# Performance work log

Hardware: AMD Instinct MI355X
Metric: run time of the kernel (lower is better)

Reference implementation:

```python
import jax, jax.numpy as jnp
import numpy as np

B, V, J, NB = 512, 6890, 24, 10
P = (J - 1) * 9  # 207 pose-blendshape features
# Standard SMPL kinematic tree (parents[0] = -1 for root)
PARENTS = np.array([-1, 0, 0, 0, 1, 2, 3, 4, 5, 6, 7, 8, 9, 9, 9, 12, 13, 14, 16, 17, 18, 19, 20, 21])


def rodrigues(aa):
    """Axis-angle [N,3] -> rotation matrices [N,3,3] (batch_rodrigues)."""
    angle = jnp.linalg.norm(aa, axis=-1, keepdims=True) + 1e-8
    axis = aa / angle
    x, y, z = axis[..., 0], axis[..., 1], axis[..., 2]
    zero = jnp.zeros_like(x)
    K = jnp.stack([zero, -z, y, z, zero, -x, -y, x, zero], axis=-1).reshape(aa.shape[0], 3, 3)
    s = jnp.sin(angle)[..., None]
    c = jnp.cos(angle)[..., None]
    return jnp.eye(3, dtype=aa.dtype) + s * K + (1.0 - c) * jnp.matmul(K, K)


def setup_inputs() -> dict:
    key = jax.random.key(0)
    ks = jax.random.split(key, 9)
    J_reg = jax.random.uniform(ks[7], (J, V), dtype=jnp.float32)
    J_reg = J_reg / jnp.sum(J_reg, axis=1, keepdims=True)
    W = jax.nn.softmax(4.0 * jax.random.normal(ks[8], (V, J), dtype=jnp.float32), axis=-1)
    return {
        "betas": jax.random.normal(ks[0], (B, NB), dtype=jnp.float32),
        "body_pose": 0.3 * jax.random.normal(ks[1], (B, (J - 1) * 3), dtype=jnp.float32),
        "global_orient": 0.3 * jax.random.normal(ks[2], (B, 3), dtype=jnp.float32),
        "transl": jax.random.normal(ks[3], (B, 3), dtype=jnp.float32),
        "v_template": jax.random.normal(ks[4], (V, 3), dtype=jnp.float32),
        "shapedirs": 0.01 * jax.random.normal(ks[5], (V, 3, NB), dtype=jnp.float32),
        "posedirs": 0.01 * jax.random.normal(ks[6], (P, V * 3), dtype=jnp.float32),
        "J_regressor": J_reg,
        "lbs_weights": W,
    }


def reference(betas, body_pose, global_orient, transl, v_template, shapedirs, posedirs, J_regressor, lbs_weights):
    b = betas.shape[0]
    # --- pose to rotation matrices (pose2rot=True path) ---
    full_pose = jnp.concatenate([global_orient, body_pose], axis=-1)  # [B, 72]
    rot_mats = rodrigues(full_pose.reshape(-1, 3)).reshape(b, J, 3, 3)
    # --- shape blend shapes ---
    v_shaped = v_template + jnp.einsum('bl,vcl->bvc', betas, shapedirs)  # [B,V,3]
    joints = jnp.einsum('jv,bvc->bjc', J_regressor, v_shaped)            # [B,J,3]
    # --- pose blend shapes ---
    pose_feature = (rot_mats[:, 1:] - jnp.eye(3, dtype=rot_mats.dtype)).reshape(b, P)
    v_posed = v_shaped + (pose_feature @ posedirs).reshape(b, V, 3)
    # --- kinematic chain (batch_rigid_transform) ---
    rel_joints = joints.at[:, 1:].add(-joints[:, PARENTS[1:]])
    top = jnp.concatenate([rot_mats, rel_joints[..., None]], axis=-1)   # [B,J,3,4]
    bottom = jnp.broadcast_to(jnp.array([0.0, 0.0, 0.0, 1.0], dtype=rot_mats.dtype), (b, J, 1, 4))
    mats = jnp.concatenate([top, bottom], axis=-2)                      # [B,J,4,4]
    chain = [mats[:, 0]]
    for i in range(1, J):  # fixed 24-joint serial composition
        chain.append(chain[PARENTS[i]] @ mats[:, i])
    A = jnp.stack(chain, axis=1)                                        # [B,J,4,4]
    posed_joints = A[..., :3, 3]
    # remove rest-pose joint locations from the transforms
    t_rel = A[..., :3, 3] - jnp.einsum('bjmn,bjn->bjm', A[..., :3, :3], joints)
    A_rel = A.at[..., :3, 3].set(t_rel)
    # --- linear blend skinning ---
    T = jnp.einsum('vj,bjmn->bvmn', lbs_weights, A_rel)                 # [B,V,4,4]
    verts = jnp.einsum('bvmn,bvn->bvm', T[..., :3, :3], v_posed) + T[..., :3, 3]
    vertices = verts + transl[:, None]
    joints_out = posed_joints + transl[:, None]
    return vertices, joints_out
```

## Files before the change

### kernel.cpp

```cpp
#include <hip/hip_runtime.h>
#include <hip/hip_bf16.h>
#include <math.h>

#define Bn 512
#define Vn 6890
#define NBn 10
#define Pn 207
#define N3n 20670
#define KP 224
#define VPAD 6912

typedef __attribute__((ext_vector_type(8))) _Float16 half8;
typedef __attribute__((ext_vector_type(4))) float f32x4;

__constant__ int c_par[24] = {-1,0,0,0,1,2,3,4,5,6,7,8,9,9,9,12,13,14,16,17,18,19,20,21};
__constant__ int c_lvl[10] = {0,1,4,7,10,15,18,20,22,24};


__global__ __launch_bounds__(256) void k_prep(
    const float* __restrict__ Jreg, const float* __restrict__ vtpl,
    const float* __restrict__ sdirs, const float* __restrict__ pdirs,
    const float* __restrict__ W, float* __restrict__ part,
    _Float16* __restrict__ B_h, _Float16* __restrict__ W_h)
{
  const int tid = threadIdx.x;
  __shared__ float wred[4][33];
  __shared__ __align__(16) float tile[224][36];

  if (blockIdx.x < 192) {
    const int j = blockIdx.x % 24;
    const int chunk = blockIdx.x / 24;
    const int lane = tid & 63, wv = tid >> 6;
    const int vlo = chunk * 862;
    const int vhi = min(Vn, vlo + 862);
    float acc[33];
#pragma unroll
    for (int k = 0; k < 33; k++) acc[k] = 0.f;
    for (int v = vlo + tid; v < vhi; v += 256) {
      float w = Jreg[(size_t)j * Vn + v];
      const float* sp = sdirs + (size_t)v * 30;
#pragma unroll
      for (int c = 0; c < 3; c++) {
#pragma unroll
        for (int l = 0; l < 10; l++) acc[c*11 + l] += w * sp[c*10 + l];
        acc[c*11 + 10] += w * vtpl[v*3 + c];
      }
    }
#pragma unroll
    for (int k = 0; k < 33; k++) {
      float s = acc[k];
      for (int off = 32; off > 0; off >>= 1) s += __shfl_xor(s, off);
      if (lane == 0) wred[wv][k] = s;
    }
    __syncthreads();
    if (tid < 33) {
      float s = wred[0][tid] + wred[1][tid] + wred[2][tid] + wred[3][tid];
      int c = tid / 11, k = tid % 11;
      part[(size_t)chunk * 792 + (j*3 + c) * 11 + k] = s;
    }
  } else if (blockIdx.x < 840) {
    const int p = blockIdx.x - 192;
    const int cols0 = p * 32;
    for (int idx = tid; idx < 207 * 8; idx += 256) {
      int row = idx >> 3, cq = (idx & 7) << 2;
      int gc = cols0 + cq;
      float4 v4 = {0.f, 0.f, 0.f, 0.f};
      if (gc + 3 < N3n) {
        v4 = *(const float4*)(pdirs + (size_t)row * N3n + gc);
      } else if (gc < N3n) {
        float t[4];
#pragma unroll
        for (int e = 0; e < 4; e++) t[e] = (gc + e < N3n) ? pdirs[(size_t)row * N3n + gc + e] : 0.f;
        v4 = make_float4(t[0], t[1], t[2], t[3]);
      }
      *(float4*)&tile[row][cq] = v4;
    }
    for (int idx = tid; idx < 17 * 32; idx += 256) {
      int r = idx >> 5, cc = idx & 31;
      int k = 207 + r;
      int gc = cols0 + cc;
      float f = 0.f;
      if (gc < N3n) {
        if (k < 217)      f = sdirs[(size_t)gc * 10 + (k - 207)];
        else if (k == 217) f = (float)(_Float16)vtpl[gc];
        else if (k == 218) { float tv = vtpl[gc]; f = tv - (float)(_Float16)tv; }
      }
      tile[k][cc] = f;
    }
    __syncthreads();
    for (int idx = tid; idx < 896; idx += 256) {
      int pl = idx >> 6;
      int l  = idx & 63;
      int ntl = pl / 7, s = pl % 7;
      int colc = ntl * 16 + (l & 15);
      int kb = s * 32 + ((l >> 4) << 3);
      half8 hv;
#pragma unroll
      for (int j = 0; j < 8; j++) hv[j] = (_Float16)tile[kb + j][colc];
      *(half8*)(B_h + ((size_t)(2 * p + ntl) * 7 + s) * 512 + (size_t)l * 8) = hv;
    }
  } else {
    int idx = (blockIdx.x - 840) * 256 + tid;
    if (idx < VPAD * 32) {
      int v = idx >> 5, k = idx & 31;
      float f;
      if (v < Vn && k < 24) f = W[(size_t)v * 24 + k];
      else if (k == 24)     f = 1.0f;
      else                  f = 0.f;
      W_h[idx] = (_Float16)f;
    }
  }
}

__global__ __launch_bounds__(256) void k_pose2(
    const float* __restrict__ betas, const float* __restrict__ body_pose,
    const float* __restrict__ gorient, const float* __restrict__ transl,
    const float* __restrict__ part,
    _Float16* __restrict__ pf_h, _Float16* __restrict__ Ar_h,
    float* __restrict__ out_joints)
{
  const int tid = threadIdx.x;
  const int wave = tid >> 6;
  const int lane = tid & 63;
  const int b = blockIdx.x * 4 + wave;

  __shared__ float JS_s[720];
  __shared__ float Jt_s[72];
  __shared__ float Rs[4][24][9];
  __shared__ float jnt[4][24][3];
  __shared__ float rel[4][24][3];
  __shared__ float A_s[4][24][12];

  for (int idx = tid; idx < 792; idx += 256) {
    float s = 0.f;
#pragma unroll
    for (int y = 0; y < 8; y++) s += part[(size_t)y * 792 + idx];
    int bid = idx / 11, k = idx % 11;
    if (k < 10) JS_s[bid * 10 + k] = s;
    else        Jt_s[bid] = s;
  }

  if (lane < 24) {
    float x, y, z;
    if (lane == 0) { x = gorient[b*3+0]; y = gorient[b*3+1]; z = gorient[b*3+2]; }
    else { int o = b*69 + (lane-1)*3; x = body_pose[o]; y = body_pose[o+1]; z = body_pose[o+2]; }
    float ang = sqrtf(x*x + y*y + z*z) + 1e-8f;
    float inv = 1.0f / ang;
    float ux = x*inv, uy = y*inv, uz = z*inv;
    float s = sinf(ang), cc = cosf(ang), omc = 1.0f - cc;
    float K[9] = {0.f, -uz, uy,  uz, 0.f, -ux,  -uy, ux, 0.f};
#pragma unroll
    for (int mm = 0; mm < 3; mm++)
#pragma unroll
      for (int nn = 0; nn < 3; nn++) {
        float kk = K[mm*3+0]*K[0+nn] + K[mm*3+1]*K[3+nn] + K[mm*3+2]*K[6+nn];
        float eye = (mm == nn) ? 1.0f : 0.0f;
        Rs[wave][lane][mm*3+nn] = eye + s*K[mm*3+nn] + omc*kk;
      }
  }
  __syncthreads();

  for (int idx = lane; idx < 72; idx += 64) {
    float a = Jt_s[idx];
#pragma unroll
    for (int l = 0; l < 10; l++) a += betas[b*10 + l] * JS_s[idx*10 + l];
    jnt[wave][idx/3][idx%3] = a;
  }
  for (int idx = lane; idx < KP; idx += 64) {
    float f = 0.f;
    if (idx < Pn) {
      int j = 1 + idx / 9, e = idx % 9;
      float eye = (e == 0 || e == 4 || e == 8) ? 1.0f : 0.0f;
      f = Rs[wave][j][e] - eye;
    } else if (idx < 217) {
      f = betas[b*10 + (idx - 207)];
    } else if (idx < 219) {
      f = 1.0f;
    }
    pf_h[(size_t)b * KP + idx] = (_Float16)f;
  }
  __syncthreads();
  for (int idx = lane; idx < 72; idx += 64) {
    int j = idx/3, cc = idx%3;
    float r = jnt[wave][j][cc];
    if (j > 0) r -= jnt[wave][c_par[j]][cc];
    rel[wave][j][cc] = r;
  }
  __syncthreads();
  if (lane < 12) {
    int m = lane/4, nn = lane%4;
    A_s[wave][0][lane] = (nn < 3) ? Rs[wave][0][m*3+nn] : rel[wave][0][m];
  }
  __syncthreads();
  for (int lev = 1; lev <= 8; lev++) {
    const int s0 = c_lvl[lev], s1 = c_lvl[lev + 1];
    const int jj = lane / 12, r = lane % 12;
    if (jj < s1 - s0) {
      const int i = s0 + jj;
      const int p = c_par[i];
      const int m = r >> 2, nn = r & 3;
      float v;
      if (nn < 3)
        v = A_s[wave][p][m*4+0]*Rs[wave][i][0+nn] + A_s[wave][p][m*4+1]*Rs[wave][i][3+nn] + A_s[wave][p][m*4+2]*Rs[wave][i][6+nn];
      else
        v = A_s[wave][p][m*4+0]*rel[wave][i][0] + A_s[wave][p][m*4+1]*rel[wave][i][1] + A_s[wave][p][m*4+2]*rel[wave][i][2] + A_s[wave][p][m*4+3];
      A_s[wave][i][r] = v;
    }
    __syncthreads();
  }
  for (int idx = lane; idx < 72; idx += 64) {
    int j = idx/3, cc = idx%3;
    out_joints[(size_t)b * 72 + idx] = A_s[wave][j][cc*4+3] + transl[b*3+cc];
  }
  for (int idx = lane; idx < 512; idx += 64) {
    int e = idx >> 5, k = idx & 31;
    float a = 0.f;
    if (e < 12 && k < 24) {
      int m = e >> 2, nn = e & 3;
      if (nn < 3) a = A_s[wave][k][m*4+nn];
      else a = A_s[wave][k][m*4+3] - (A_s[wave][k][m*4+0]*jnt[wave][k][0] + A_s[wave][k][m*4+1]*jnt[wave][k][1] + A_s[wave][k][m*4+2]*jnt[wave][k][2]);
    } else if (k == 24 && e < 12 && (e & 3) == 3) {
      a = transl[b*3 + (e >> 2)];
    }
    Ar_h[(size_t)b * 512 + idx] = (_Float16)a;
  }
}

__global__ __launch_bounds__(256) void k_mm5(
    const _Float16* __restrict__ pf_h, const _Float16* __restrict__ B_h,
    const _Float16* __restrict__ W_h, const _Float16* __restrict__ Ar_h,
    float* __restrict__ out)
{
  const int lin = blockIdx.x;
  const int r8 = lin & 7;
  const int k2 = lin >> 3;
  const int b_t = k2 & 15;
  const int m8 = k2 >> 4;
  const int v_t = r8 * 14 + m8;
  if (v_t >= 108) return;

  const int tid = threadIdx.x;
  const int l = tid & 63;
  const int wave = tid >> 6;
  const int b0 = b_t * 32;
  const int v0 = v_t * 64;

  __shared__ __align__(16) float vpT[192 * 32];

  const int c0 = l & 15;
  const int kk0 = (l >> 4) << 3;
  const int ntb = v_t * 12 + wave * 3;
  f32x4 acc[2][3];
#pragma unroll
  for (int t = 0; t < 2; t++)
#pragma unroll
    for (int n = 0; n < 3; n++) acc[t][n] = (f32x4){0.f, 0.f, 0.f, 0.f};

#pragma unroll
  for (int s = 0; s < 7; s++) {
    half8 bv[3];
#pragma unroll
    for (int n = 0; n < 3; n++)
      bv[n] = *(const half8*)(B_h + ((size_t)(ntb + n) * 7 + s) * 512 + l * 8);
#pragma unroll
    for (int t = 0; t < 2; t++) {
      half8 fa = *(const half8*)(pf_h + (size_t)(b0 + t * 16 + c0) * KP + kk0 + s * 32);
#pragma unroll
      for (int n = 0; n < 3; n++)
        acc[t][n] = __builtin_amdgcn_mfma_f32_16x16x32_f16(fa, bv[n], acc[t][n], 0, 0, 0);
    }
  }
  {
    const int rowq = (l >> 4) * 4;
#pragma unroll
    for (int t = 0; t < 2; t++)
#pragma unroll
      for (int n = 0; n < 3; n++) {
        const int col = wave * 48 + n * 16 + c0;
        const int rowb = t * 16 + rowq;
        *(f32x4*)&vpT[col * 32 + (rowb ^ ((col & 7) << 2))] = acc[t][n];
      }
  }
  __syncthreads();

  const int c = c0;
  const int g = l >> 4;
  const int kk = g << 3;

  half8 wh[4], ah[8];
#pragma unroll
  for (int mt = 0; mt < 4; mt++)
    wh[mt] = *(const half8*)(W_h + (size_t)(v0 + mt * 16 + c) * 32 + kk);
#pragma unroll
  for (int i = 0; i < 8; i++)
    ah[i] = *(const half8*)(Ar_h + (size_t)(b0 + wave * 8 + i) * 512 + c * 32 + kk);

#pragma unroll
  for (int mt = 0; mt < 4; mt++) {
    const int vl2 = mt * 16 + c;
    const int v = v0 + vl2;
    const bool ok = (g < 3) && (v < Vn);
    const int colx = 3 * vl2, coly = colx + 1, colz = colx + 2;
#pragma unroll
    for (int q = 0; q < 2; q++) {
      const int rb = wave * 8 + q * 4;
      f32x4 X = *(const f32x4*)&vpT[colx * 32 + (rb ^ ((colx & 7) << 2))];
      f32x4 Y = *(const f32x4*)&vpT[coly * 32 + (rb ^ ((coly & 7) << 2))];
      f32x4 Z = *(const f32x4*)&vpT[colz * 32 + (rb ^ ((colz & 7) << 2))];
#pragma unroll
      for (int r = 0; r < 4; r++) {
        f32x4 t = {0.f, 0.f, 0.f, 0.f};
        t = __builtin_amdgcn_mfma_f32_16x16x32_f16(ah[q * 4 + r], wh[mt], t, 0, 0, 0);
        if (ok) {
          const int bl = wave * 8 + q * 4 + r;
          out[((size_t)(b0 + bl) * Vn + v) * 3 + g] = t[0]*X[r] + t[1]*Y[r] + t[2]*Z[r] + t[3];
        }
      }
    }
  }
}


__global__ __launch_bounds__(256) void k_jsjt_part(
    const float* __restrict__ Jreg, const float* __restrict__ vtpl,
    const float* __restrict__ sdirs, float* __restrict__ part)
{
  const int bid = blockIdx.x;
  const int chunk = blockIdx.y;
  const int j = bid / 3, c = bid % 3;
  const int tid = threadIdx.x;
  const int vlo = chunk * 862;
  const int vhi = min(Vn, vlo + 862);
  float acc[11];
#pragma unroll
  for (int k = 0; k < 11; k++) acc[k] = 0.f;
  for (int v = vlo + tid; v < vhi; v += 256) {
    float w = Jreg[(size_t)j * Vn + v];
    int n = v * 3 + c;
#pragma unroll
    for (int l = 0; l < 10; l++) acc[l] += w * sdirs[(size_t)n * 10 + l];
    acc[10] += w * vtpl[n];
  }
  __shared__ float red[256];
  for (int k = 0; k < 11; k++) {
    red[tid] = acc[k];
    __syncthreads();
    for (int s = 128; s > 0; s >>= 1) {
      if (tid < s) red[tid] += red[tid + s];
      __syncthreads();
    }
    if (tid == 0) part[(size_t)chunk * 792 + bid * 11 + k] = red[0];
    __syncthreads();
  }
}

__global__ __launch_bounds__(1024) void k_jsjt_red(
    const float* __restrict__ part, float* __restrict__ JS, float* __restrict__ Jt)
{
  const int t = threadIdx.x;
  if (t >= 792) return;
  float s = 0.f;
#pragma unroll
  for (int y = 0; y < 8; y++) s += part[(size_t)y * 792 + t];
  int bid = t / 11, k = t % 11;
  if (k < 10) JS[bid * 10 + k] = s;
  else        Jt[bid] = s;
}

__global__ __launch_bounds__(64) void k_pose_fb(
    const float* __restrict__ betas, const float* __restrict__ body_pose,
    const float* __restrict__ gorient, const float* __restrict__ transl,
    const float* __restrict__ JS, const float* __restrict__ Jt,
    float* __restrict__ pf_ws, float* __restrict__ Ar_ws,
    float* __restrict__ out_joints)
{
  const int b = blockIdx.x;
  const int tid = threadIdx.x;
  __shared__ float Rs[24][9];
  __shared__ float jnt[24][3];
  __shared__ float rel[24][3];
  __shared__ float A_s[24][12];

  if (tid < 24) {
    float x, y, z;
    if (tid == 0) { x = gorient[b*3+0]; y = gorient[b*3+1]; z = gorient[b*3+2]; }
    else { int o = b*69 + (tid-1)*3; x = body_pose[o]; y = body_pose[o+1]; z = body_pose[o+2]; }
    float ang = sqrtf(x*x + y*y + z*z) + 1e-8f;
    float inv = 1.0f / ang;
    float ux = x*inv, uy = y*inv, uz = z*inv;
    float s = sinf(ang), cc = cosf(ang), omc = 1.0f - cc;
    float K[9] = {0.f, -uz, uy,  uz, 0.f, -ux,  -uy, ux, 0.f};
#pragma unroll
    for (int mm = 0; mm < 3; mm++)
#pragma unroll
      for (int nn = 0; nn < 3; nn++) {
        float kk = K[mm*3+0]*K[0+nn] + K[mm*3+1]*K[3+nn] + K[mm*3+2]*K[6+nn];
        float eye = (mm == nn) ? 1.0f : 0.0f;
        Rs[tid][mm*3+nn] = eye + s*K[mm*3+nn] + omc*kk;
      }
  }
  for (int idx = tid; idx < 72; idx += 64) {
    float a = Jt[idx];
#pragma unroll
    for (int l = 0; l < 10; l++) a += betas[b*10 + l] * JS[idx*10 + l];
    jnt[idx/3][idx%3] = a;
  }
  __syncthreads();
  for (int idx = tid; idx < Pn; idx += 64) {
    int j = 1 + idx / 9, e = idx % 9;
    float eye = (e == 0 || e == 4 || e == 8) ? 1.0f : 0.0f;
    pf_ws[(size_t)b * Pn + idx] = Rs[j][e] - eye;
  }
  for (int idx = tid; idx < 72; idx += 64) {
    int j = idx/3, cc = idx%3;
    float r = jnt[j][cc];
    if (j > 0) r -= jnt[c_par[j]][cc];
    rel[j][cc] = r;
  }
  __syncthreads();
  if (tid < 12) {
    int m = tid/4, nn = tid%4;
    A_s[0][tid] = (nn < 3) ? Rs[0][m*3+nn] : rel[0][m];
  }
  __syncthreads();
  for (int i = 1; i < 24; i++) {
    if (tid < 12) {
      int m = tid/4, nn = tid%4;
      int p = c_par[i];
      float v;
      if (nn < 3)
        v = A_s[p][m*4+0]*Rs[i][0+nn] + A_s[p][m*4+1]*Rs[i][3+nn] + A_s[p][m*4+2]*Rs[i][6+nn];
      else
        v = A_s[p][m*4+0]*rel[i][0] + A_s[p][m*4+1]*rel[i][1] + A_s[p][m*4+2]*rel[i][2] + A_s[p][m*4+3];
      A_s[i][tid] = v;
    }
    __syncthreads();
  }
  for (int idx = tid; idx < 72; idx += 64) {
    int j = idx/3, cc = idx%3;
    out_joints[(size_t)b * 72 + idx] = A_s[j][cc*4+3] + transl[b*3+cc];
  }
  for (int idx = tid; idx < 288; idx += 64) {
    int j = idx/12, r = idx%12, m = r/4, nn = r%4;
    float v;
    if (nn < 3) v = A_s[j][m*4+nn];
    else v = A_s[j][m*4+3] - (A_s[j][m*4+0]*jnt[j][0] + A_s[j][m*4+1]*jnt[j][1] + A_s[j][m*4+2]*jnt[j][2]);
    Ar_ws[(size_t)b * 288 + idx] = v;
  }
}

__global__ __launch_bounds__(192) void k_verts_fb(
    const float* __restrict__ betas, const float* __restrict__ transl,
    const float* __restrict__ vtpl, const float* __restrict__ sdirs,
    const float* __restrict__ pdirs, const float* __restrict__ W,
    const float* __restrict__ pf_ws, const float* __restrict__ Ar_ws,
    float* __restrict__ out)
{
  const int tid = threadIdx.x;
  const int b0 = blockIdx.x * 16;
  const int v0 = blockIdx.y * 128;
  const int n0 = v0 * 3;
  __shared__ __align__(16) float pf_s[Pn][16];
  __shared__ __align__(16) float Ar_s[16][288];
  __shared__ __align__(16) float vp_s[16][384];
  __shared__ float betas_s[16][NBn];
  __shared__ float transl_s[16][3];
  for (int idx = tid; idx < Pn * 16; idx += 192) {
    int p = idx >> 4, bi = idx & 15;
    pf_s[p][bi] = pf_ws[(size_t)(b0 + bi) * Pn + p];
  }
  for (int idx = tid; idx < 16 * 288; idx += 192)
    Ar_s[idx / 288][idx % 288] = Ar_ws[(size_t)b0 * 288 + idx];
  for (int idx = tid; idx < 16 * NBn; idx += 192)
    betas_s[idx / NBn][idx % NBn] = betas[(size_t)b0 * NBn + idx];
  for (int idx = tid; idx < 48; idx += 192)
    transl_s[idx / 3][idx % 3] = transl[(size_t)b0 * 3 + idx];
  __syncthreads();
  const int n = n0 + 2 * tid;
  const bool valid = (n < N3n);
  float acc0[16], acc1[16];
#pragma unroll
  for (int i = 0; i < 16; i++) { acc0[i] = 0.f; acc1[i] = 0.f; }
  for (int p = 0; p < Pn; p++) {
    float pd0 = 0.f, pd1 = 0.f;
    if (valid) { float2 t = *(const float2*)(pdirs + (size_t)p * N3n + n); pd0 = t.x; pd1 = t.y; }
    const float4* row = (const float4*)(pf_s[p]);
#pragma unroll
    for (int q = 0; q < 4; q++) {
      float4 f = row[q];
      acc0[4*q+0] += f.x * pd0;  acc1[4*q+0] += f.x * pd1;
      acc0[4*q+1] += f.y * pd0;  acc1[4*q+1] += f.y * pd1;
      acc0[4*q+2] += f.z * pd0;  acc1[4*q+2] += f.z * pd1;
      acc0[4*q+3] += f.w * pd0;  acc1[4*q+3] += f.w * pd1;
    }
  }
  float sd0[10], sd1[10], vt0 = 0.f, vt1 = 0.f;
#pragma unroll
  for (int l = 0; l < 10; l++) { sd0[l] = 0.f; sd1[l] = 0.f; }
  if (valid) {
    for (int l = 0; l < 10; l++) { sd0[l] = sdirs[(size_t)n*10 + l]; sd1[l] = sdirs[(size_t)n*10 + 10 + l]; }
    vt0 = vtpl[n]; vt1 = vtpl[n+1];
  }
#pragma unroll
  for (int bi = 0; bi < 16; bi++) {
    float s0 = vt0, s1 = vt1;
#pragma unroll
    for (int l = 0; l < 10; l++) { float bb = betas_s[bi][l]; s0 += bb*sd0[l]; s1 += bb*sd1[l]; }
    acc0[bi] += s0; acc1[bi] += s1;
  }
#pragma unroll
  for (int bi = 0; bi < 16; bi++) { vp_s[bi][2*tid] = acc0[bi]; vp_s[bi][2*tid+1] = acc1[bi]; }
  __syncthreads();
  const int m = tid / 64;
  const int vl = tid % 64;
  const int va = v0 + vl, vb = v0 + vl + 64;
  const bool va_ok = (va < Vn), vb_ok = (vb < Vn);
  float Wr0[24], Wr1[24];
#pragma unroll
  for (int j = 0; j < 24; j++) { Wr0[j] = 0.f; Wr1[j] = 0.f; }
  if (va_ok) { const float4* wp = (const float4*)(W + (size_t)va*24);
#pragma unroll
    for (int q = 0; q < 6; q++) { float4 f = wp[q]; Wr0[4*q]=f.x; Wr0[4*q+1]=f.y; Wr0[4*q+2]=f.z; Wr0[4*q+3]=f.w; } }
  if (vb_ok) { const float4* wp = (const float4*)(W + (size_t)vb*24);
#pragma unroll
    for (int q = 0; q < 6; q++) { float4 f = wp[q]; Wr1[4*q]=f.x; Wr1[4*q+1]=f.y; Wr1[4*q+2]=f.z; Wr1[4*q+3]=f.w; } }
  for (int bi = 0; bi < 16; bi++) {
    float Ta0=0.f,Ta1=0.f,Ta2=0.f,Ta3=0.f, Tb0=0.f,Tb1=0.f,Tb2=0.f,Tb3=0.f;
    const float4* arb = (const float4*)(Ar_s[bi]);
#pragma unroll
    for (int j = 0; j < 24; j++) {
      float4 a = arb[j*3 + m];
      float wa = Wr0[j], wb = Wr1[j];
      Ta0 += wa*a.x; Ta1 += wa*a.y; Ta2 += wa*a.z; Ta3 += wa*a.w;
      Tb0 += wb*a.x; Tb1 += wb*a.y; Tb2 += wb*a.z; Tb3 += wb*a.w;
    }
    float tr = transl_s[bi][m];
    if (va_ok) {
      float x = vp_s[bi][vl*3+0], y = vp_s[bi][vl*3+1], z = vp_s[bi][vl*3+2];
      out[((size_t)(b0+bi)*Vn + va)*3 + m] = Ta0*x + Ta1*y + Ta2*z + Ta3 + tr;
    }
    if (vb_ok) {
      float x = vp_s[bi][(vl+64)*3+0], y = vp_s[bi][(vl+64)*3+1], z = vp_s[bi][(vl+64)*3+2];
      out[((size_t)(b0+bi)*Vn + vb)*3 + m] = Tb0*x + Tb1*y + Tb2*z + Tb3 + tr;
    }
  }
}

extern "C" void kernel_launch(void* const* d_in, const int* in_sizes, int n_in,
                              void* d_out, int out_size, void* d_ws, size_t ws_size,
                              hipStream_t stream)
{
  const float *betas=nullptr, *bpose=nullptr, *gorient=nullptr, *transl=nullptr,
              *vtpl=nullptr, *sdirs=nullptr, *pdirs=nullptr, *Jreg=nullptr, *W=nullptr;
  int seen1536 = 0, seen165360 = 0;
  for (int i = 0; i < n_in; i++) {
    const float* p = (const float*)d_in[i];
    switch (in_sizes[i]) {
      case 5120:    betas = p; break;
      case 35328:   bpose = p; break;
      case 20670:   vtpl  = p; break;
      case 206700:  sdirs = p; break;
      case 4278690: pdirs = p; break;
      case 1536:    if (seen1536++ == 0) gorient = p; else transl = p; break;
      case 165360:  if (seen165360++ == 0) Jreg = p; else W = p; break;
      default: break;
    }
  }
  float* out = (float*)d_out;

  float* ws   = (float*)d_ws;
  float* part = ws;
  float* JS   = ws + 6336;
  float* Jt   = ws + 7056;
  float* pf   = ws + 7128;
  float* Ar   = ws + 113112;
  _Float16* pf_h = (_Float16*)(ws + 260568);
  _Float16* B_h  = (_Float16*)(ws + 317912);
  _Float16* W_h  = (_Float16*)(ws + 2640344);
  _Float16* Ar_h = (_Float16*)(ws + 2861528);
  const size_t WS_NEED = (size_t)3123672 * 4;
  const bool big = (ws_size >= WS_NEED);

  if (big) {
    k_prep<<<1704, 256, 0, stream>>>(Jreg, vtpl, sdirs, pdirs, W, part, B_h, W_h);
    k_pose2<<<128, 256, 0, stream>>>(betas, bpose, gorient, transl, part,
                                     pf_h, Ar_h, out + (size_t)Bn * Vn * 3);
    k_mm5<<<1792, 256, 0, stream>>>(pf_h, B_h, W_h, Ar_h, out);
  } else {
    k_jsjt_part<<<dim3(72, 8), 256, 0, stream>>>(Jreg, vtpl, sdirs, part);
    k_jsjt_red<<<1, 1024, 0, stream>>>(part, JS, Jt);
    k_pose_fb<<<Bn, 64, 0, stream>>>(betas, bpose, gorient, transl, JS, Jt, pf, Ar,
                                     out + (size_t)Bn * Vn * 3);
    k_verts_fb<<<dim3(32, 54), 192, 0, stream>>>(betas, transl, vtpl, sdirs,
                                                 pdirs, W, pf, Ar, out);
  }
}
```

Baseline: 53.32 us.

## Repack skinning transforms so each MFMA covers four batches and drops padding rows

The per-batch fp16 skinning-transform matrix is now laid out in groups of four batches, ordered by output row m, with 4 batches × 4 columns packed into each 16-row MFMA operand. The old layout used 16 rows, of which only 12 were real and the g==3 lanes were masked. Each skinning MFMA now yields three useful output components (m loop) across four batches, and no quarter of the lanes is wasted. The goal is fewer MFMAs and Ar loads in the LBS epilogue and fewer idle lanes, at the cost of scalar LDS reads of vertex positions and a new index mapping that must stay consistent between producer and consumer.

```diff
diff --git a/kernel.cpp b/kernel.cpp
--- a/kernel.cpp
+++ b/kernel.cpp
@@ -212,21 +212,22 @@
     int j = idx/3, cc = idx%3;
     out_joints[(size_t)b * 72 + idx] = A_s[wave][j][cc*4+3] + transl[b*3+cc];
   }
-  for (int idx = lane; idx < 512; idx += 64) {
-    int e = idx >> 5, k = idx & 31;
+  for (int idx = lane; idx < 384; idx += 64) {
+    int m = idx >> 7;
+    int j = (idx >> 5) & 3;
+    int k = idx & 31;
     float a = 0.f;
-    if (e < 12 && k < 24) {
-      int m = e >> 2, nn = e & 3;
-      if (nn < 3) a = A_s[wave][k][m*4+nn];
+    if (k < 24) {
+      if (j < 3) a = A_s[wave][k][m*4+j];
       else a = A_s[wave][k][m*4+3] - (A_s[wave][k][m*4+0]*jnt[wave][k][0] + A_s[wave][k][m*4+1]*jnt[wave][k][1] + A_s[wave][k][m*4+2]*jnt[wave][k][2]);
-    } else if (k == 24 && e < 12 && (e & 3) == 3) {
-      a = transl[b*3 + (e >> 2)];
-    }
-    Ar_h[(size_t)b * 512 + idx] = (_Float16)a;
-  }
-}
-
-__global__ __launch_bounds__(256) void k_mm5(
+    } else if (k == 24 && j == 3) {
+      a = transl[b*3 + m];
+    }
+    Ar_h[(size_t)(b >> 2) * 1536 + m * 512 + ((b & 3) * 4 + j) * 32 + k] = (_Float16)a;
+  }
+}
+
+__global__ __launch_bounds__(256) void k_mm7(
     const _Float16* __restrict__ pf_h, const _Float16* __restrict__ B_h,
     const _Float16* __restrict__ W_h, const _Float16* __restrict__ Ar_h,
     float* __restrict__ out)
@@ -283,38 +284,41 @@
   }
   __syncthreads();
 
-  const int c = c0;
   const int g = l >> 4;
   const int kk = g << 3;
 
-  half8 wh[4], ah[8];
+  half8 wh[4];
 #pragma unroll
   for (int mt = 0; mt < 4; mt++)
-    wh[mt] = *(const half8*)(W_h + (size_t)(v0 + mt * 16 + c) * 32 + kk);
-#pragma unroll
-  for (int i = 0; i < 8; i++)
-    ah[i] = *(const half8*)(Ar_h + (size_t)(b0 + wave * 8 + i) * 512 + c * 32 + kk);
+    wh[mt] = *(const half8*)(W_h + (size_t)(v0 + mt * 16 + c0) * 32 + kk);
+
+  half8 aq[2][3];
+#pragma unroll
+  for (int q2 = 0; q2 < 2; q2++) {
+    const size_t qb = (size_t)(b_t * 8 + wave * 2 + q2) * 1536;
+#pragma unroll
+    for (int m = 0; m < 3; m++)
+      aq[q2][m] = *(const half8*)(Ar_h + qb + m * 512 + c0 * 32 + kk);
+  }
 
 #pragma unroll
   for (int mt = 0; mt < 4; mt++) {
-    const int vl2 = mt * 16 + c;
+    const int vl2 = mt * 16 + c0;
     const int v = v0 + vl2;
-    const bool ok = (g < 3) && (v < Vn);
+    const bool ok = (v < Vn);
     const int colx = 3 * vl2, coly = colx + 1, colz = colx + 2;
 #pragma unroll
-    for (int q = 0; q < 2; q++) {
-      const int rb = wave * 8 + q * 4;
-      f32x4 X = *(const f32x4*)&vpT[colx * 32 + (rb ^ ((colx & 7) << 2))];
-      f32x4 Y = *(const f32x4*)&vpT[coly * 32 + (rb ^ ((coly & 7) << 2))];
-      f32x4 Z = *(const f32x4*)&vpT[colz * 32 + (rb ^ ((colz & 7) << 2))];
-#pragma unroll
-      for (int r = 0; r < 4; r++) {
+    for (int q2 = 0; q2 < 2; q2++) {
+      const int bl = wave * 8 + q2 * 4 + g;
+      float x = vpT[colx * 32 + (bl ^ ((colx & 7) << 2))];
+      float y = vpT[coly * 32 + (bl ^ ((coly & 7) << 2))];
+      float z = vpT[colz * 32 + (bl ^ ((colz & 7) << 2))];
+      const size_t ob = ((size_t)(b0 + bl) * Vn + v) * 3;
+#pragma unroll
+      for (int m = 0; m < 3; m++) {
         f32x4 t = {0.f, 0.f, 0.f, 0.f};
-        t = __builtin_amdgcn_mfma_f32_16x16x32_f16(ah[q * 4 + r], wh[mt], t, 0, 0, 0);
-        if (ok) {
-          const int bl = wave * 8 + q * 4 + r;
-          out[((size_t)(b0 + bl) * Vn + v) * 3 + g] = t[0]*X[r] + t[1]*Y[r] + t[2]*Z[r] + t[3];
-        }
+        t = __builtin_amdgcn_mfma_f32_16x16x32_f16(aq[q2][m], wh[mt], t, 0, 0, 0);
+        if (ok) out[ob + m] = t[0]*x + t[1]*y + t[2]*z + t[3];
       }
     }
   }
@@ -585,7 +589,7 @@
     k_prep<<<1704, 256, 0, stream>>>(Jreg, vtpl, sdirs, pdirs, W, part, B_h, W_h);
     k_pose2<<<128, 256, 0, stream>>>(betas, bpose, gorient, transl, part,
                                      pf_h, Ar_h, out + (size_t)Bn * Vn * 3);
-    k_mm5<<<1792, 256, 0, stream>>>(pf_h, B_h, W_h, Ar_h, out);
+    k_mm7<<<1792, 256, 0, stream>>>(pf_h, B_h, W_h, Ar_h, out);
   } else {
     k_jsjt_part<<<dim3(72, 8), 256, 0, stream>>>(Jreg, vtpl, sdirs, part);
     k_jsjt_red<<<1, 1024, 0, stream>>>(part, JS, Jt);
```

Measured after the change: 55.18 us. 1.03x slower.
